# Kernel tuning notes

Measured on AMD Instinct MI355X. Metric: run time of the kernel, lower is better.

The kernel has to match this reference:

```python
import jax, jax.numpy as jnp
import numpy as np

N, E, IN, HID, H, G, CLS = 20000, 160000, 128, 96, 6, 512, 128
HD = H * HID  # heads * out_channels = 576
ARC_S = 30.0  # ArcFace scale (no margin at inference, no labels passed)


def _lin_params(key, fan_in, fan_out):
    k1, k2 = jax.random.split(key)
    lim = 1.0 / np.sqrt(fan_in)
    W = jax.random.uniform(k1, (fan_in, fan_out), minval=-lim, maxval=lim, dtype=jnp.float32)
    b = jax.random.uniform(k2, (fan_out,), minval=-lim, maxval=lim, dtype=jnp.float32)
    return W, b


def setup_inputs() -> dict:
    key = jax.random.key(0)
    ks = jax.random.split(key, 32)
    x = jax.random.normal(ks[0], (N, IN), dtype=jnp.float32)
    edge_index = jax.random.randint(ks[1], (2, E), 0, N, dtype=jnp.int64)
    batch = jnp.sort(jax.random.randint(ks[2], (N,), 0, G, dtype=jnp.int64))
    # conv1: IN -> HID (per-head dim HID, H heads)
    Wq1, bq1 = _lin_params(ks[3], IN, HD)
    Wk1, bk1 = _lin_params(ks[4], IN, HD)
    Wv1, bv1 = _lin_params(ks[5], IN, HD)
    Ws1, bs1 = _lin_params(ks[6], IN, HID)
    # convs 2..5 share shapes: HID -> HID, stacked on leading axis of 4
    def stack(fn_keys, fi, fo):
        Ws, bs = zip(*[_lin_params(k, fi, fo) for k in fn_keys])
        return jnp.stack(Ws), jnp.stack(bs)
    Wq_r, bq_r = stack(ks[7:11], HID, HD)
    Wk_r, bk_r = stack(ks[11:15], HID, HD)
    Wv_r, bv_r = stack(ks[15:19], HID, HD)
    Ws_r, bs_r = stack(ks[19:23], HID, HID)
    fc1_w, fc1_b = _lin_params(ks[23], HID, HID)
    fc2_w, fc2_b = _lin_params(ks[24], HID, HID)
    arc_w = jax.random.normal(ks[25], (CLS, HID), dtype=jnp.float32)
    return dict(x=x, edge_index=edge_index, batch=batch,
                Wq1=Wq1, bq1=bq1, Wk1=Wk1, bk1=bk1, Wv1=Wv1, bv1=bv1, Ws1=Ws1, bs1=bs1,
                Wq_r=Wq_r, bq_r=bq_r, Wk_r=Wk_r, bk_r=bk_r, Wv_r=Wv_r, bv_r=bv_r,
                Ws_r=Ws_r, bs_r=bs_r,
                fc1_w=fc1_w, fc1_b=fc1_b, fc2_w=fc2_w, fc2_b=fc2_b, arc_w=arc_w)


def transformer_conv(x, src, dst, Wq, bq, Wk, bk, Wv, bv, Ws, bs):
    n = x.shape[0]
    q = (x @ Wq + bq).reshape(n, H, HID)
    k = (x @ Wk + bk).reshape(n, H, HID)
    v = (x @ Wv + bv).reshape(n, H, HID)
    # edge-wise attention logits [E, H]
    alpha = jnp.einsum('ehd,ehd->eh', q[dst], k[src]) / jnp.sqrt(jnp.float32(HID))
    # segment softmax over incoming edges of each destination node
    m = jax.ops.segment_max(alpha, dst, num_segments=n)
    a = jnp.exp(alpha - m[dst])
    s = jax.ops.segment_sum(a, dst, num_segments=n)
    a = a / s[dst]
    out = jax.ops.segment_sum(a[:, :, None] * v[src], dst, num_segments=n)  # [n, H, HID]
    # concat=False -> mean over heads; root_weight skip connection
    return out.mean(axis=1) + x @ Ws + bs


def reference(x, edge_index, batch,
              Wq1, bq1, Wk1, bk1, Wv1, bv1, Ws1, bs1,
              Wq_r, bq_r, Wk_r, bk_r, Wv_r, bv_r, Ws_r, bs_r,
              fc1_w, fc1_b, fc2_w, fc2_b, arc_w):
    src, dst = edge_index[0], edge_index[1]
    h = jax.nn.relu(transformer_conv(x, src, dst, Wq1, bq1, Wk1, bk1, Wv1, bv1, Ws1, bs1))
    for i in range(4):  # gtconv2..gtconv5
        h = jax.nn.relu(transformer_conv(h, src, dst, Wq_r[i], bq_r[i], Wk_r[i], bk_r[i],
                                         Wv_r[i], bv_r[i], Ws_r[i], bs_r[i]))
    # global mean pool over graphs
    sums = jax.ops.segment_sum(h, batch, num_segments=G)
    cnt = jax.ops.segment_sum(jnp.ones((h.shape[0], 1), h.dtype), batch, num_segments=G)
    g = sums / jnp.maximum(cnt, 1.0)
    g = jax.nn.relu(g @ fc1_w + fc1_b)
    g = jax.nn.relu(g @ fc2_w + fc2_b)
    # ArcFace without labels: scaled cosine logits
    gn = g / (jnp.linalg.norm(g, axis=-1, keepdims=True) + 1e-12)
    wn = arc_w / (jnp.linalg.norm(arc_w, axis=-1, keepdims=True) + 1e-12)
    return ARC_S * (gn @ wn.T)
```

## Files before the change

### kernel.cpp

```cpp
#include <hip/hip_runtime.h>
#include <math.h>

#define N_NODES 20000
#define N_EDGES 160000
#define DIM_IN  128
#define HIDDEN  96
#define NH      6
#define HD      576
#define LDROW   704
#define KVF8LD  1152
#define NALL    1824
#define NGRAPH  512
#define NCLS    128
#define CHUNK   32
#define SLD     104
#define BSTR    112

typedef unsigned short ushort_t;
typedef unsigned char uchar_t;
typedef __attribute__((ext_vector_type(8))) short bf16x8;
typedef __attribute__((ext_vector_type(4))) float f32x4;
typedef __attribute__((ext_vector_type(2))) float f32x2;

static __device__ __forceinline__ ushort_t f2bf(float f) {
    unsigned int u = __float_as_uint(f);
    return (ushort_t)((u + 0x7fffu + ((u >> 16) & 1u)) >> 16);
}
static __device__ __forceinline__ float bfs(ushort_t u) { return __uint_as_float((unsigned int)u << 16); }
static __device__ __forceinline__ float bflo(unsigned int u) { return __uint_as_float(u << 16); }
static __device__ __forceinline__ float bfhi(unsigned int u) { return __uint_as_float(u & 0xffff0000u); }

#define PREP_CVT_BLOCKS 10000
#define PREP_DEG_BLOCKS 625
#define PREP_GB_BLOCKS  3
__global__ void k_prep(const float* __restrict__ x, ushort_t* __restrict__ xb,
                       const int* __restrict__ edst, int* __restrict__ deg,
                       const int* __restrict__ batch, int* __restrict__ gbound)
{
    int b = blockIdx.x;
    if (b < PREP_CVT_BLOCKS) {
        int i = b * 256 + threadIdx.x;
        if (i < N_NODES * DIM_IN) xb[i] = f2bf(x[i]);
    } else if (b < PREP_CVT_BLOCKS + PREP_DEG_BLOCKS) {
        int e = (b - PREP_CVT_BLOCKS) * 256 + threadIdx.x;
        if (e < N_EDGES) atomicAdd(&deg[edst[e]], 1);
    } else {
        int g = (b - PREP_CVT_BLOCKS - PREP_DEG_BLOCKS) * 256 + threadIdx.x;
        if (g <= NGRAPH) {
            int lo = 0, hi = N_NODES;
            while (lo < hi) {
                int mid = (lo + hi) >> 1;
                if (batch[mid] < g) lo = mid + 1; else hi = mid;
            }
            gbound[g] = lo;
        }
    }
}

__global__ void k_cvt_wT_all(
    const float* __restrict__ Wq1, const float* __restrict__ Wk1,
    const float* __restrict__ Wv1, const float* __restrict__ Ws1,
    const float* __restrict__ Wq_r, const float* __restrict__ Wk_r,
    const float* __restrict__ Wv_r, const float* __restrict__ Ws_r,
    ushort_t* __restrict__ Wb0, ushort_t* __restrict__ Wbr)
{
    const int L = blockIdx.y;
    const int K = (L == 0) ? DIM_IN : HIDDEN;
    int i = blockIdx.x * blockDim.x + threadIdx.x;
    if (i >= K * NALL) return;
    const float *Wq, *Wk, *Wv, *Ws; ushort_t* dst;
    if (L == 0) { Wq = Wq1; Wk = Wk1; Wv = Wv1; Ws = Ws1; dst = Wb0; }
    else {
        int j = L - 1;
        Wq = Wq_r + (size_t)j * HIDDEN * HD; Wk = Wk_r + (size_t)j * HIDDEN * HD;
        Wv = Wv_r + (size_t)j * HIDDEN * HD; Ws = Ws_r + (size_t)j * HIDDEN * HIDDEN;
        dst = Wbr + (size_t)j * HIDDEN * NALL;
    }
    int n = i / K, k = i - n * K;
    float v;
    if (n < 576)       v = Wq[(size_t)k * HD + n];
    else if (n < 1152) v = Wk[(size_t)k * HD + (n - 576)];
    else if (n < 1728) v = Wv[(size_t)k * HD + (n - 1152)];
    else               v = Ws[(size_t)k * HIDDEN + (n - 1728)];
    dst[i] = f2bf(v);
}

template<int KDIM>
__global__ __launch_bounds__(256) void gemm_qkvs_mfma(
    const ushort_t* __restrict__ A, int M,
    const ushort_t* __restrict__ WbT,
    const float* __restrict__ bq, const float* __restrict__ bk,
    const float* __restrict__ bv, const float* __restrict__ bs,
    ushort_t* __restrict__ kvqs, uchar_t* __restrict__ kvf8)
{
    constexpr int LDB = KDIM + 8;
    constexpr int K8  = KDIM >> 3;
    __shared__ __align__(16) ushort_t smem[128 * SLD];
    const int t    = threadIdx.x;
    const int lane = t & 63;
    const int w    = t >> 6;
    const int wm   = w & 1, wn = w >> 1;
    const int quad = lane >> 4;
    const int l16  = lane & 15;
    const int m0   = blockIdx.y * 128;
    const int rb   = blockIdx.x;
    const int n0   = rb * 96;

    for (int idx = t; idx < 96 * K8; idx += 256) {
        int c = idx / K8, kc = idx - c * K8;
        uint4 v = *(const uint4*)(WbT + (size_t)(n0 + c) * KDIM + kc * 8);
        *(uint4*)(&smem[c * LDB + kc * 8]) = v;
    }

    const ushort_t* Arow[4];
    #pragma unroll
    for (int i = 0; i < 4; i++) {
        int row = m0 + wm * 64 + i * 16 + l16;
        row = min(row, M - 1);
        Arow[i] = A + (size_t)row * KDIM + quad * 8;
    }
    __syncthreads();

    f32x4 acc[4][3] = {};
    #pragma unroll
    for (int ks = 0; ks < KDIM; ks += 32) {
        bf16x8 af[4], bfv[3];
        #pragma unroll
        for (int i = 0; i < 4; i++) af[i] = *(const bf16x8*)(Arow[i] + ks);
        #pragma unroll
        for (int j = 0; j < 3; j++)
            bfv[j] = *(const bf16x8*)(&smem[(wn * 48 + j * 16 + l16) * LDB + ks + quad * 8]);
        #pragma unroll
        for (int i = 0; i < 4; i++)
            #pragma unroll
            for (int j = 0; j < 3; j++)
                acc[i][j] = __builtin_amdgcn_mfma_f32_16x16x32_bf16(af[i], bfv[j], acc[i][j], 0, 0, 0);
    }

    int region; const float* biasp;
    if (rb < 6)       { region = 0; biasp = bq; }
    else if (rb < 12) { region = 1; biasp = bk; }
    else if (rb < 18) { region = 2; biasp = bv; }
    else              { region = 3; biasp = bs; }
    const int colbase = (region == 3) ? 0 : (rb - region * 6) * 96;
    float bj[3];
    #pragma unroll
    for (int j = 0; j < 3; j++) bj[j] = biasp[colbase + wn * 48 + j * 16 + l16];

    __syncthreads();

    if (region == 1 || region == 2) {
        uchar_t* bstage = (uchar_t*)smem;
        #pragma unroll
        for (int i = 0; i < 4; i++) {
            #pragma unroll
            for (int r = 0; r < 4; r++) {
                int row = wm * 64 + i * 16 + quad * 4 + r;
                #pragma unroll
                for (int j = 0; j < 3; j++) {
                    float v = acc[i][j][r] + bj[j];
                    int pk = __builtin_amdgcn_cvt_pk_fp8_f32(v, v, 0, false);
                    bstage[row * BSTR + wn * 48 + j * 16 + l16] = (uchar_t)(pk & 0xff);
                }
            }
        }
        __syncthreads();
        const int c0 = (rb - 6) * 96;
        for (int idx = t; idx < 128 * 6; idx += 256) {
            int r = idx / 6, v4 = idx - r * 6;
            int row = m0 + r;
            if (row < M)
                *(uint4*)(kvf8 + (size_t)row * KVF8LD + c0 + v4 * 16) =
                    *(const uint4*)(bstage + r * BSTR + v4 * 16);
        }
    } else {
        int dstoff = (region == 0) ? n0 : 576;
        #pragma unroll
        for (int i = 0; i < 4; i++) {
            #pragma unroll
            for (int r = 0; r < 4; r++) {
                int row = wm * 64 + i * 16 + quad * 4 + r;
                #pragma unroll
                for (int j = 0; j < 3; j++)
                    smem[row * SLD + wn * 48 + j * 16 + l16] = f2bf(acc[i][j][r] + bj[j]);
            }
        }
        __syncthreads();
        for (int idx = t; idx < 128 * 12; idx += 256) {
            int r = idx / 12, v = idx - r * 12;
            int row = m0 + r;
            if (row < M)
                *(uint4*)(kvqs + (size_t)row * LDROW + dstoff + v * 8) =
                    *(const uint4*)(&smem[r * SLD + v * 8]);
        }
    }
}

__global__ __launch_bounds__(1024) void k_scan(const int* __restrict__ deg,
                                               int* __restrict__ row_ptr,
                                               int* __restrict__ cursor)
{
    __shared__ int part[1024];
    int t = threadIdx.x;
    const int chunk = (N_NODES + 1023) / 1024;
    int b = t * chunk;
    int s = 0;
    for (int i = 0; i < chunk; i++)
        if (b + i < N_NODES) s += deg[b + i];
    part[t] = s;
    __syncthreads();
    for (int o = 1; o < 1024; o <<= 1) {
        int v = (t >= o) ? part[t - o] : 0;
        __syncthreads();
        part[t] += v;
        __syncthreads();
    }
    int run = part[t] - s;
    for (int i = 0; i < chunk; i++) {
        if (b + i < N_NODES) {
            row_ptr[b + i] = run;
            cursor[b + i]  = run;
            run += deg[b + i];
        }
    }
    if (t == 1023) row_ptr[N_NODES] = part[1023];
}

__global__ void k_scatter(const int* __restrict__ esrc, const int* __restrict__ edst,
                          int* __restrict__ cursor, int* __restrict__ csrc)
{
    int e = blockIdx.x * blockDim.x + threadIdx.x;
    if (e < N_EDGES) {
        int pos = atomicAdd(&cursor[edst[e]], 1);
        csrc[pos] = esrc[e];
    }
}

__global__ __launch_bounds__(192) void node_attn(
    const ushort_t* __restrict__ kvqs, const uchar_t* __restrict__ kvf8,
    const int* __restrict__ row_ptr, const int* __restrict__ csrc,
    ushort_t* __restrict__ hb)
{
    const int n = blockIdx.x;
    const int t = threadIdx.x;
    const int lane = t & 31;
    const int g = t >> 5;
    const int el = lane >> 2;
    const int qr = lane & 3;

    __shared__ float Qs[HD];
    __shared__ float wbuf[CHUNK * NH];
    __shared__ int   srcs[CHUNK];
    __shared__ float m[NH], l[NH], scale[NH], linv[NH];
    __shared__ float arr[HD];

    const int beg = row_ptr[n], end = row_ptr[n + 1];
    const ushort_t* qk = kvqs + (size_t)n * LDROW;

    if (t < 72) {
        uint4 v = *(const uint4*)(qk + t * 8);
        unsigned int uu[4] = {v.x, v.y, v.z, v.w};
        #pragma unroll
        for (int j = 0; j < 4; j++) {
            Qs[t * 8 + 2 * j]     = bflo(uu[j]);
            Qs[t * 8 + 2 * j + 1] = bfhi(uu[j]);
        }
    }
    if (t < NH) { m[t] = -1e30f; l[t] = 0.f; }

    const int d4 = 4 * t;
    const int hh = d4 / HIDDEN;
    float a[4] = {0.f, 0.f, 0.f, 0.f};
    const float qa = 0.10206207261596577f;
    const uchar_t* vbase = kvf8 + 576 + d4;

    for (int cb = beg; cb < end; cb += CHUNK) {
        const int c = min(CHUNK, end - cb);
        __syncthreads();
        if (t < c) srcs[t] = csrc[cb + t];
        __syncthreads();

        unsigned int vpre[8];
        if (t < 144) {
            #pragma unroll
            for (int j = 0; j < 8; j++) {
                int e = min(j, c - 1);
                vpre[j] = *(const unsigned int*)(vbase + (size_t)srcs[e] * KVF8LD);
            }
        }

        for (int eb = 0; eb < c; eb += 8) {
            int e8 = eb + el;
            bool act = e8 < c;
            int src = srcs[act ? e8 : 0];
            const uchar_t* kp = kvf8 + (size_t)src * KVF8LD + g * HIDDEN + qr * 24;
            uint2 a0 = *(const uint2*)(kp);
            uint2 a1 = *(const uint2*)(kp + 8);
            uint2 a2 = *(const uint2*)(kp + 16);
            const float* qb = &Qs[g * HIDDEN + qr * 24];
            unsigned int uu[6] = {a0.x, a0.y, a1.x, a1.y, a2.x, a2.y};
            float p = 0.f;
            #pragma unroll
            for (int k2 = 0; k2 < 6; k2++) {
                f32x2 lo = __builtin_amdgcn_cvt_pk_f32_fp8(uu[k2], false);
                f32x2 hi = __builtin_amdgcn_cvt_pk_f32_fp8(uu[k2], true);
                p += lo[0] * qb[4 * k2]     + lo[1] * qb[4 * k2 + 1]
                   + hi[0] * qb[4 * k2 + 2] + hi[1] * qb[4 * k2 + 3];
            }
            p += __shfl_xor(p, 1, 32);
            p += __shfl_xor(p, 2, 32);
            if (act && qr == 0) wbuf[e8 * NH + g] = p * qa;
        }
        __syncthreads();

        {
            float logit = (lane < c) ? wbuf[lane * NH + g] : -1e30f;
            float cm = logit;
            #pragma unroll
            for (int o = 16; o; o >>= 1) cm = fmaxf(cm, __shfl_xor(cm, o, 32));
            cm = fmaxf(cm, m[g]);
            float wv = (lane < c) ? __expf(logit - cm) : 0.f;
            if (lane < c) wbuf[lane * NH + g] = wv;
            float lp = wv;
            #pragma unroll
            for (int o = 16; o; o >>= 1) lp += __shfl_xor(lp, o, 32);
            if (lane == 0) {
                float sc = __expf(m[g] - cm);
                scale[g] = sc;
                l[g] = l[g] * sc + lp;
                m[g] = cm;
            }
        }
        __syncthreads();

        if (t < 144) {
            float sc = scale[hh];
            #pragma unroll
            for (int j = 0; j < 4; j++) a[j] *= sc;
            #pragma unroll
            for (int j = 0; j < 8; j++) {
                if (j < c) {
                    float w2 = wbuf[j * NH + hh];
                    f32x2 lo = __builtin_amdgcn_cvt_pk_f32_fp8(vpre[j], false);
                    f32x2 hi = __builtin_amdgcn_cvt_pk_f32_fp8(vpre[j], true);
                    a[0] += w2 * lo[0];
                    a[1] += w2 * lo[1];
                    a[2] += w2 * hi[0];
                    a[3] += w2 * hi[1];
                }
            }
            int e = 8;
            for (; e + 4 <= c; e += 4) {
                unsigned int r[4];
                #pragma unroll
                for (int j = 0; j < 4; j++)
                    r[j] = *(const unsigned int*)(vbase + (size_t)srcs[e + j] * KVF8LD);
                #pragma unroll
                for (int j = 0; j < 4; j++) {
                    float w2 = wbuf[(e + j) * NH + hh];
                    f32x2 lo = __builtin_amdgcn_cvt_pk_f32_fp8(r[j], false);
                    f32x2 hi = __builtin_amdgcn_cvt_pk_f32_fp8(r[j], true);
                    a[0] += w2 * lo[0];
                    a[1] += w2 * lo[1];
                    a[2] += w2 * hi[0];
                    a[3] += w2 * hi[1];
                }
            }
            for (; e < c; e++) {
                unsigned int r = *(const unsigned int*)(vbase + (size_t)srcs[e] * KVF8LD);
                float w2 = wbuf[e * NH + hh];
                f32x2 lo = __builtin_amdgcn_cvt_pk_f32_fp8(r, false);
                f32x2 hi = __builtin_amdgcn_cvt_pk_f32_fp8(r, true);
                a[0] += w2 * lo[0];
                a[1] += w2 * lo[1];
                a[2] += w2 * hi[0];
                a[3] += w2 * hi[1];
            }
        }
    }

    if (t < NH) linv[t] = (l[t] > 0.f) ? 1.0f / l[t] : 0.f;
    __syncthreads();
    if (t < 144) {
        float li = linv[hh];
        #pragma unroll
        for (int j = 0; j < 4; j++) arr[d4 + j] = a[j] * li;
    }
    __syncthreads();

    if (t < HIDDEN) {
        float s = (arr[t] + arr[HIDDEN + t] + arr[2 * HIDDEN + t] +
                   arr[3 * HIDDEN + t] + arr[4 * HIDDEN + t] + arr[5 * HIDDEN + t])
                  * (1.0f / 6.0f);
        s += bfs(qk[576 + t]);
        s = fmaxf(s, 0.0f);
        hb[n * HIDDEN + t] = f2bf(s);
    }
}

__global__ __launch_bounds__(128) void k_head(
    const ushort_t* __restrict__ hb, const int* __restrict__ gbound,
    const float* __restrict__ fc1w, const float* __restrict__ fc1b,
    const float* __restrict__ fc2w, const float* __restrict__ fc2b,
    const float* __restrict__ arcw, float* __restrict__ out)
{
    int g = blockIdx.x, t = threadIdx.x;
    __shared__ float v0[HIDDEN], v1[HIDDEN], v2[HIDDEN];
    __shared__ float gnorm;
    const int s0 = gbound[g], s1 = gbound[g + 1];
    float cnt = fmaxf((float)(s1 - s0), 1.0f);
    if (t < HIDDEN) {
        float s = 0.f;
        for (int n = s0; n < s1; n++) s += bfs(hb[(size_t)n * HIDDEN + t]);
        v0[t] = s / cnt;
    }
    __syncthreads();
    if (t < HIDDEN) {
        float s = fc1b[t];
        for (int k = 0; k < HIDDEN; k++) s += v0[k] * fc1w[k * HIDDEN + t];
        v1[t] = fmaxf(s, 0.f);
    }
    __syncthreads();
    if (t < HIDDEN) {
        float s = fc2b[t];
        for (int k = 0; k < HIDDEN; k++) s += v1[k] * fc2w[k * HIDDEN + t];
        v2[t] = fmaxf(s, 0.f);
    }
    __syncthreads();
    if (t == 0) {
        float s = 0.f;
        for (int k = 0; k < HIDDEN; k++) s += v2[k] * v2[k];
        gnorm = sqrtf(s) + 1e-12f;
    }
    __syncthreads();
    if (t < NCLS) {
        float dot = 0.f, wn = 0.f;
        const float* wr = arcw + (size_t)t * HIDDEN;
        for (int k = 0; k < HIDDEN; k++) {
            float w = wr[k];
            dot += w * v2[k];
            wn  += w * w;
        }
        out[g * NCLS + t] = 30.0f * dot / (gnorm * (sqrtf(wn) + 1e-12f));
    }
}

extern "C" void kernel_launch(void* const* d_in, const int* in_sizes, int n_in,
                              void* d_out, int out_size, void* d_ws, size_t ws_size,
                              hipStream_t stream)
{
    (void)in_sizes; (void)n_in; (void)out_size; (void)ws_size;

    const float* x     = (const float*)d_in[0];
    const int*   ei    = (const int*)d_in[1];
    const int*   batch = (const int*)d_in[2];
    const float* Wq1 = (const float*)d_in[3];  const float* bq1 = (const float*)d_in[4];
    const float* Wk1 = (const float*)d_in[5];  const float* bk1 = (const float*)d_in[6];
    const float* Wv1 = (const float*)d_in[7];  const float* bv1 = (const float*)d_in[8];
    const float* Ws1 = (const float*)d_in[9];  const float* bs1 = (const float*)d_in[10];
    const float* Wq_r = (const float*)d_in[11]; const float* bq_r = (const float*)d_in[12];
    const float* Wk_r = (const float*)d_in[13]; const float* bk_r = (const float*)d_in[14];
    const float* Wv_r = (const float*)d_in[15]; const float* bv_r = (const float*)d_in[16];
    const float* Ws_r = (const float*)d_in[17]; const float* bs_r = (const float*)d_in[18];
    const float* fc1w = (const float*)d_in[19]; const float* fc1b = (const float*)d_in[20];
    const float* fc2w = (const float*)d_in[21]; const float* fc2b = (const float*)d_in[22];
    const float* arcw = (const float*)d_in[23];
    float* out = (float*)d_out;

    const int* esrc = ei;
    const int* edst = ei + N_EDGES;

    char* base = (char*)d_ws;
    size_t off = 0;
    auto alloc = [&](size_t bytes) -> void* {
        off = (off + 255) & ~(size_t)255;
        void* p = base + off;
        off += bytes;
        return p;
    };
    ushort_t* kvqs = (ushort_t*)alloc((size_t)N_NODES * LDROW * 2);
    uchar_t*  kvf8 = (uchar_t*)alloc((size_t)N_NODES * KVF8LD);
    ushort_t* xb  = (ushort_t*)alloc((size_t)N_NODES * DIM_IN * 2);
    ushort_t* hb0 = (ushort_t*)alloc((size_t)N_NODES * HIDDEN * 2);
    ushort_t* hb1 = (ushort_t*)alloc((size_t)N_NODES * HIDDEN * 2);
    ushort_t* Wb0 = (ushort_t*)alloc((size_t)DIM_IN * NALL * 2);
    ushort_t* Wbr = (ushort_t*)alloc((size_t)4 * HIDDEN * NALL * 2);
    int*   deg     = (int*)alloc(N_NODES * 4);
    int*   row_ptr = (int*)alloc((N_NODES + 1) * 4);
    int*   cursor  = (int*)alloc(N_NODES * 4);
    int*   csrc    = (int*)alloc(N_EDGES * 4);
    int*   gbound  = (int*)alloc((NGRAPH + 1) * 4);

    hipMemsetAsync(deg, 0, N_NODES * 4, stream);
    k_prep<<<PREP_CVT_BLOCKS + PREP_DEG_BLOCKS + PREP_GB_BLOCKS, 256, 0, stream>>>(
        x, xb, edst, deg, batch, gbound);
    {
        dim3 gw((DIM_IN * NALL + 255) / 256, 5);
        k_cvt_wT_all<<<gw, 256, 0, stream>>>(Wq1, Wk1, Wv1, Ws1,
                                             Wq_r, Wk_r, Wv_r, Ws_r, Wb0, Wbr);
    }
    k_scan<<<1, 1024, 0, stream>>>(deg, row_ptr, cursor);
    k_scatter<<<(N_EDGES + 255) / 256, 256, 0, stream>>>(esrc, edst, cursor, csrc);

    const ushort_t* Ain = xb;
    ushort_t* hbcur = hb0;
    for (int L = 0; L < 5; L++) {
        const ushort_t* Wb = (L == 0) ? Wb0 : (Wbr + (size_t)(L - 1) * HIDDEN * NALL);
        const float *bq, *bk, *bv, *bs;
        if (L == 0) { bq = bq1; bk = bk1; bv = bv1; bs = bs1; }
        else {
            int i = L - 1;
            bq = bq_r + (size_t)i * HD; bk = bk_r + (size_t)i * HD;
            bv = bv_r + (size_t)i * HD; bs = bs_r + (size_t)i * HIDDEN;
        }
        dim3 g(19, (N_NODES + 127) / 128);
        if (L == 0)
            gemm_qkvs_mfma<DIM_IN><<<g, 256, 0, stream>>>(Ain, N_NODES, Wb,
                                                          bq, bk, bv, bs, kvqs, kvf8);
        else
            gemm_qkvs_mfma<HIDDEN><<<g, 256, 0, stream>>>(Ain, N_NODES, Wb,
                                                          bq, bk, bv, bs, kvqs, kvf8);
        node_attn<<<N_NODES, 192, 0, stream>>>(kvqs, kvf8, row_ptr, csrc, hbcur);
        Ain = hbcur;
        hbcur = (hbcur == hb0) ? hb1 : hb0;
    }

    k_head<<<NGRAPH, 128, 0, stream>>>(hbcur == hb0 ? hb1 : hb0, gbound,
                                       fc1w, fc1b, fc2w, fc2b, arcw, out);
}
```

Before: 529.7 us.

## Shrink node attention to one wavefront per node with wider per-lane V accumulation

```diff
diff --git a/kernel.cpp b/kernel.cpp
--- a/kernel.cpp
+++ b/kernel.cpp
@@ -236,68 +236,73 @@
     }
 }
 
-__global__ __launch_bounds__(192) void node_attn(
+__global__ __launch_bounds__(64) void node_attn(
     const ushort_t* __restrict__ kvqs, const uchar_t* __restrict__ kvf8,
     const int* __restrict__ row_ptr, const int* __restrict__ csrc,
     ushort_t* __restrict__ hb)
 {
-    const int n = blockIdx.x;
-    const int t = threadIdx.x;
-    const int lane = t & 31;
-    const int g = t >> 5;
-    const int el = lane >> 2;
-    const int qr = lane & 3;
-
-    __shared__ float Qs[HD];
+    const int n    = blockIdx.x;
+    const int lane = threadIdx.x;
+
+    __shared__ float QA[HD];
     __shared__ float wbuf[CHUNK * NH];
     __shared__ int   srcs[CHUNK];
-    __shared__ float m[NH], l[NH], scale[NH], linv[NH];
-    __shared__ float arr[HD];
+    __shared__ float mh[NH], lh[NH], scl[NH], linv[NH];
 
     const int beg = row_ptr[n], end = row_ptr[n + 1];
     const ushort_t* qk = kvqs + (size_t)n * LDROW;
 
-    if (t < 72) {
-        uint4 v = *(const uint4*)(qk + t * 8);
+    {
+        uint4 v = *(const uint4*)(qk + lane * 8);
         unsigned int uu[4] = {v.x, v.y, v.z, v.w};
         #pragma unroll
         for (int j = 0; j < 4; j++) {
-            Qs[t * 8 + 2 * j]     = bflo(uu[j]);
-            Qs[t * 8 + 2 * j + 1] = bfhi(uu[j]);
-        }
-    }
-    if (t < NH) { m[t] = -1e30f; l[t] = 0.f; }
-
-    const int d4 = 4 * t;
-    const int hh = d4 / HIDDEN;
-    float a[4] = {0.f, 0.f, 0.f, 0.f};
+            QA[lane * 8 + 2 * j]     = bflo(uu[j]);
+            QA[lane * 8 + 2 * j + 1] = bfhi(uu[j]);
+        }
+        if (lane < 8) {
+            uint4 v2 = *(const uint4*)(qk + (64 + lane) * 8);
+            unsigned int uu2[4] = {v2.x, v2.y, v2.z, v2.w};
+            #pragma unroll
+            for (int j = 0; j < 4; j++) {
+                QA[(64 + lane) * 8 + 2 * j]     = bflo(uu2[j]);
+                QA[(64 + lane) * 8 + 2 * j + 1] = bfhi(uu2[j]);
+            }
+        }
+    }
+    if (lane < NH) { mh[lane] = -1e30f; lh[lane] = 0.f; }
+
+    const int sub = lane >> 5;
+    const int h32 = lane & 31;
+    const int g   = h32 >> 2;
+    const int gg  = (g < 6) ? g : 0;
+    const int qr  = h32 & 3;
+    const int hh  = lane >> 3;
+    const int j8  = lane & 7;
+    const uchar_t* vb = kvf8 + 576 + ((hh < 6) ? hh : 0) * HIDDEN + j8 * 12;
+
+    float acc[12];
+    #pragma unroll
+    for (int d = 0; d < 12; d++) acc[d] = 0.f;
     const float qa = 0.10206207261596577f;
-    const uchar_t* vbase = kvf8 + 576 + d4;
+
+    __syncthreads();
 
     for (int cb = beg; cb < end; cb += CHUNK) {
         const int c = min(CHUNK, end - cb);
-        __syncthreads();
-        if (t < c) srcs[t] = csrc[cb + t];
-        __syncthreads();
-
-        unsigned int vpre[8];
-        if (t < 144) {
-            #pragma unroll
-            for (int j = 0; j < 8; j++) {
-                int e = min(j, c - 1);
-                vpre[j] = *(const unsigned int*)(vbase + (size_t)srcs[e] * KVF8LD);
-            }
-        }
-
-        for (int eb = 0; eb < c; eb += 8) {
-            int e8 = eb + el;
-            bool act = e8 < c;
-            int src = srcs[act ? e8 : 0];
-            const uchar_t* kp = kvf8 + (size_t)src * KVF8LD + g * HIDDEN + qr * 24;
+        if (lane < c) srcs[lane] = csrc[cb + lane];
+        __syncthreads();
+
+        #pragma unroll 2
+        for (int eb = 0; eb < c; eb += 2) {
+            int e = eb + sub;
+            bool act = (e < c) && (g < 6);
+            int src = srcs[(e < c) ? e : 0];
+            const uchar_t* kp = kvf8 + (size_t)src * KVF8LD + gg * HIDDEN + qr * 24;
             uint2 a0 = *(const uint2*)(kp);
             uint2 a1 = *(const uint2*)(kp + 8);
             uint2 a2 = *(const uint2*)(kp + 16);
-            const float* qb = &Qs[g * HIDDEN + qr * 24];
+            const float* qb = &QA[gg * HIDDEN + qr * 24];
             unsigned int uu[6] = {a0.x, a0.y, a1.x, a1.y, a2.x, a2.y};
             float p = 0.f;
             #pragma unroll
@@ -307,94 +312,112 @@
                 p += lo[0] * qb[4 * k2]     + lo[1] * qb[4 * k2 + 1]
                    + hi[0] * qb[4 * k2 + 2] + hi[1] * qb[4 * k2 + 3];
             }
-            p += __shfl_xor(p, 1, 32);
-            p += __shfl_xor(p, 2, 32);
-            if (act && qr == 0) wbuf[e8 * NH + g] = p * qa;
-        }
-        __syncthreads();
-
-        {
-            float logit = (lane < c) ? wbuf[lane * NH + g] : -1e30f;
+            p += __shfl_xor(p, 1, 64);
+            p += __shfl_xor(p, 2, 64);
+            if (act && qr == 0) wbuf[e * NH + g] = p * qa;
+        }
+        __syncthreads();
+
+        #pragma unroll
+        for (int s = 0; s < 3; s++) {
+            int h = 2 * s + sub;
+            float logit = (h32 < c) ? wbuf[h32 * NH + h] : -1e30f;
             float cm = logit;
             #pragma unroll
             for (int o = 16; o; o >>= 1) cm = fmaxf(cm, __shfl_xor(cm, o, 32));
-            cm = fmaxf(cm, m[g]);
-            float wv = (lane < c) ? __expf(logit - cm) : 0.f;
-            if (lane < c) wbuf[lane * NH + g] = wv;
+            cm = fmaxf(cm, mh[h]);
+            float wv = (h32 < c) ? __expf(logit - cm) : 0.f;
+            if (h32 < c) wbuf[h32 * NH + h] = wv;
             float lp = wv;
             #pragma unroll
             for (int o = 16; o; o >>= 1) lp += __shfl_xor(lp, o, 32);
-            if (lane == 0) {
-                float sc = __expf(m[g] - cm);
-                scale[g] = sc;
-                l[g] = l[g] * sc + lp;
-                m[g] = cm;
-            }
-        }
-        __syncthreads();
-
-        if (t < 144) {
-            float sc = scale[hh];
-            #pragma unroll
-            for (int j = 0; j < 4; j++) a[j] *= sc;
-            #pragma unroll
-            for (int j = 0; j < 8; j++) {
-                if (j < c) {
-                    float w2 = wbuf[j * NH + hh];
-                    f32x2 lo = __builtin_amdgcn_cvt_pk_f32_fp8(vpre[j], false);
-                    f32x2 hi = __builtin_amdgcn_cvt_pk_f32_fp8(vpre[j], true);
-                    a[0] += w2 * lo[0];
-                    a[1] += w2 * lo[1];
-                    a[2] += w2 * hi[0];
-                    a[3] += w2 * hi[1];
+            if (h32 == 0) {
+                float sc = __expf(mh[h] - cm);
+                scl[h] = sc;
+                lh[h] = lh[h] * sc + lp;
+                mh[h] = cm;
+            }
+        }
+        __syncthreads();
+
+        if (lane < 48) {
+            float sc = scl[hh];
+            #pragma unroll
+            for (int d = 0; d < 12; d++) acc[d] *= sc;
+            int e = 0;
+            for (; e + 2 <= c; e += 2) {
+                int s0 = srcs[e], s1 = srcs[e + 1];
+                const uchar_t* p0 = vb + (size_t)s0 * KVF8LD;
+                const uchar_t* p1 = vb + (size_t)s1 * KVF8LD;
+                unsigned int r0[3], r1[3];
+                #pragma unroll
+                for (int k = 0; k < 3; k++) {
+                    r0[k] = *(const unsigned int*)(p0 + 4 * k);
+                    r1[k] = *(const unsigned int*)(p1 + 4 * k);
                 }
-            }
-            int e = 8;
-            for (; e + 4 <= c; e += 4) {
-                unsigned int r[4];
+                float w0 = wbuf[e * NH + hh], w1 = wbuf[(e + 1) * NH + hh];
                 #pragma unroll
-                for (int j = 0; j < 4; j++)
-                    r[j] = *(const unsigned int*)(vbase + (size_t)srcs[e + j] * KVF8LD);
+                for (int k = 0; k < 3; k++) {
+                    f32x2 lo0 = __builtin_amdgcn_cvt_pk_f32_fp8(r0[k], false);
+                    f32x2 hi0 = __builtin_amdgcn_cvt_pk_f32_fp8(r0[k], true);
+                    acc[4 * k]     += w0 * lo0[0];
+                    acc[4 * k + 1] += w0 * lo0[1];
+                    acc[4 * k + 2] += w0 * hi0[0];
+                    acc[4 * k + 3] += w0 * hi0[1];
+                    f32x2 lo1 = __builtin_amdgcn_cvt_pk_f32_fp8(r1[k], false);
+                    f32x2 hi1 = __builtin_amdgcn_cvt_pk_f32_fp8(r1[k], true);
+                    acc[4 * k]     += w1 * lo1[0];
+                    acc[4 * k + 1] += w1 * lo1[1];
+                    acc[4 * k + 2] += w1 * hi1[0];
+                    acc[4 * k + 3] += w1 * hi1[1];
+                }
+            }
+            if (e < c) {
+                int s0 = srcs[e];
+                const uchar_t* p0 = vb + (size_t)s0 * KVF8LD;
+                float w0 = wbuf[e * NH + hh];
                 #pragma unroll
-                for (int j = 0; j < 4; j++) {
-                    float w2 = wbuf[(e + j) * NH + hh];
-                    f32x2 lo = __builtin_amdgcn_cvt_pk_f32_fp8(r[j], false);
-                    f32x2 hi = __builtin_amdgcn_cvt_pk_f32_fp8(r[j], true);
-                    a[0] += w2 * lo[0];
-                    a[1] += w2 * lo[1];
-                    a[2] += w2 * hi[0];
-                    a[3] += w2 * hi[1];
+                for (int k = 0; k < 3; k++) {
+                    unsigned int r = *(const unsigned int*)(p0 + 4 * k);
+                    f32x2 lo = __builtin_amdgcn_cvt_pk_f32_fp8(r, false);
+                    f32x2 hi = __builtin_amdgcn_cvt_pk_f32_fp8(r, true);
+                    acc[4 * k]     += w0 * lo[0];
+                    acc[4 * k + 1] += w0 * lo[1];
+                    acc[4 * k + 2] += w0 * hi[0];
+                    acc[4 * k + 3] += w0 * hi[1];
                 }
             }
-            for (; e < c; e++) {
-                unsigned int r = *(const unsigned int*)(vbase + (size_t)srcs[e] * KVF8LD);
-                float w2 = wbuf[e * NH + hh];
-                f32x2 lo = __builtin_amdgcn_cvt_pk_f32_fp8(r, false);
-                f32x2 hi = __builtin_amdgcn_cvt_pk_f32_fp8(r, true);
-                a[0] += w2 * lo[0];
-                a[1] += w2 * lo[1];
-                a[2] += w2 * hi[0];
-                a[3] += w2 * hi[1];
-            }
-        }
-    }
-
-    if (t < NH) linv[t] = (l[t] > 0.f) ? 1.0f / l[t] : 0.f;
-    __syncthreads();
-    if (t < 144) {
+        }
+        __syncthreads();
+    }
+
+    if (lane < NH) linv[lane] = (lh[lane] > 0.f) ? 1.0f / lh[lane] : 0.f;
+    __syncthreads();
+    if (lane < 48) {
         float li = linv[hh];
         #pragma unroll
-        for (int j = 0; j < 4; j++) arr[d4 + j] = a[j] * li;
-    }
-    __syncthreads();
-
-    if (t < HIDDEN) {
-        float s = (arr[t] + arr[HIDDEN + t] + arr[2 * HIDDEN + t] +
-                   arr[3 * HIDDEN + t] + arr[4 * HIDDEN + t] + arr[5 * HIDDEN + t])
+        for (int d = 0; d < 12; d++)
+            QA[hh * HIDDEN + j8 * 12 + d] = acc[d] * li;
+    }
+    __syncthreads();
+
+    {
+        int d = lane;
+        float s = (QA[d] + QA[HIDDEN + d] + QA[2 * HIDDEN + d] +
+                   QA[3 * HIDDEN + d] + QA[4 * HIDDEN + d] + QA[5 * HIDDEN + d])
                   * (1.0f / 6.0f);
-        s += bfs(qk[576 + t]);
+        s += bfs(qk[576 + d]);
         s = fmaxf(s, 0.0f);
-        hb[n * HIDDEN + t] = f2bf(s);
+        hb[n * HIDDEN + d] = f2bf(s);
+        if (lane < 32) {
+            int d2 = 64 + lane;
+            float s2 = (QA[d2] + QA[HIDDEN + d2] + QA[2 * HIDDEN + d2] +
+                        QA[3 * HIDDEN + d2] + QA[4 * HIDDEN + d2] + QA[5 * HIDDEN + d2])
+                       * (1.0f / 6.0f);
+            s2 += bfs(qk[576 + d2]);
+            s2 = fmaxf(s2, 0.0f);
+            hb[n * HIDDEN + d2] = f2bf(s2);
+        }
     }
 }
 
@@ -520,7 +543,7 @@
         else
             gemm_qkvs_mfma<HIDDEN><<<g, 256, 0, stream>>>(Ain, N_NODES, Wb,
                                                           bq, bk, bv, bs, kvqs, kvf8);
-        node_attn<<<N_NODES, 192, 0, stream>>>(kvqs, kvf8, row_ptr, csrc, hbcur);
+        node_attn<<<N_NODES, 64, 0, stream>>>(kvqs, kvf8, row_ptr, csrc, hbcur);
         Ain = hbcur;
         hbcur = (hbcur == hb0) ? hb1 : hb0;
     }
```

New measurement: 511.7 us. 1.04x faster.
